# Optimization experiments

Hardware: AMD Instinct MI355X
Metric: run time of the kernel (lower is better)

## Reference

```python
import jax, jax.numpy as jnp
import numpy as np

MAX_FRAMES = 12
TOPK = 49
NUM_SAMPLES = 500
SIGMA = 0.05
EPS = 1e-5
NOISE_KEY = jax.random.key(1)


def _ln(x, g, b):
    m = x.mean(-1, keepdims=True)
    v = ((x - m) ** 2).mean(-1, keepdims=True)
    return (x - m) / jnp.sqrt(v + EPS) * g + b


def _gelu(x):
    return jax.nn.gelu(x, approximate=False)  # torch nn.GELU default is exact erf


def _predict(x, guid, ln_in_g, ln_in_b, W_in, ln_gd_g, ln_gd_b, W_gd, W_out1, W_out2):
    # x: (b, N, D), guid: (b, 1, D) -> score (b, N, 1)
    b, N, D = x.shape
    local = _gelu(_ln(x, ln_in_g, ln_in_b) @ W_in)            # (b, N, D/2)
    glob = _gelu(_ln(guid, ln_gd_g, ln_gd_b) @ W_gd)          # (b, 1, D/2); LN is per-token so repeat-then-LN == LN-then-broadcast
    glob = jnp.broadcast_to(glob, (b, N, glob.shape[-1]))
    h = jnp.concatenate([local, glob], axis=-1)               # (b, N, D)
    return jnp.tanh(_gelu(h @ W_out1) @ W_out2)               # (b, N, 1)


def _perturbed_topk(scores):
    # scores: (b, d) -> soft indicators (b, k, d); same math as one_hot(sorted topk idx).mean over samples,
    # computed by scatter-add instead of materializing the (b, ns, k, d) one-hot tensor.
    b, d = scores.shape
    noise = jax.random.normal(NOISE_KEY, (b, NUM_SAMPLES, d), scores.dtype)
    perturbed = scores[:, None, :] + SIGMA * noise            # (b, ns, d)
    _, idx = jax.lax.top_k(perturbed, TOPK)                   # (b, ns, k)
    idx = jnp.sort(idx, axis=-1)
    bi = jnp.arange(b)[:, None, None]
    ki = jnp.arange(TOPK)[None, None, :]
    ind = jnp.zeros((b, TOPK, d), scores.dtype).at[bi, ki, idx].add(1.0 / NUM_SAMPLES)
    return ind


def setup_inputs() -> dict:
    key = jax.random.key(0)
    ks = jax.random.split(key, 9)
    B, F, N, D = 8, MAX_FRAMES, 196, 512
    H = D // 2
    s = 0.02
    return {
        "x": jax.random.normal(ks[0], (B, F * N, D), jnp.float32),
        "guidance_frame": jax.random.normal(ks[1], (B, F, D), jnp.float32),
        "guidance_sentence": jax.random.normal(ks[2], (B, 1, D), jnp.float32),
        "ln_in_g": jnp.ones((D,), jnp.float32),
        "ln_in_b": jnp.zeros((D,), jnp.float32),
        "W_in": jax.random.normal(ks[3], (D, H), jnp.float32) * s,
        "ln_gd_g": jnp.ones((D,), jnp.float32),
        "ln_gd_b": jnp.zeros((D,), jnp.float32),
        "W_gd": jax.random.normal(ks[4], (D, H), jnp.float32) * s,
        "W_out1": jax.random.normal(ks[5], (D, H), jnp.float32) * s,
        "W_out2": jax.random.normal(ks[6], (H, 1), jnp.float32) * s,
    }


def reference(x, guidance_frame, guidance_sentence, ln_in_g, ln_in_b, W_in, ln_gd_g, ln_gd_b, W_gd, W_out1, W_out2):
    B, L, D = x.shape
    N = L // MAX_FRAMES
    xf = x.reshape(B * MAX_FRAMES, N, D)                       # (b', N, D)
    gf = guidance_frame.reshape(B * MAX_FRAMES, 1, D)
    gs = jnp.broadcast_to(guidance_sentence, (B, MAX_FRAMES, D)).reshape(B * MAX_FRAMES, 1, D)
    s1 = _predict(xf, gf, ln_in_g, ln_in_b, W_in, ln_gd_g, ln_gd_b, W_gd, W_out1, W_out2)[..., 0]
    s2 = _predict(xf, gs, ln_in_g, ln_in_b, W_in, ln_gd_g, ln_gd_b, W_gd, W_out1, W_out2)[..., 0]
    score = s1 + s2                                            # (b', N)
    ind = _perturbed_topk(score)                               # (b', k, N)
    selected = jnp.einsum('bkl,bld->bkd', ind, xf)             # (b', k, D)
    return selected.reshape(B, MAX_FRAMES, TOPK, D)
```

## Files before the change

### kernel.cpp

```cpp
#include <hip/hip_runtime.h>
#include <stdint.h>

#define DEV __device__ __forceinline__

#define BP 96
#define NTOK 196
#define DIM 512
#define HID 256
#define NS 500
#define TOPK 49
#define ROWS (BP * NTOK)
#define GBLK (ROWS / 32)
#define SPB 10
#define CNTSZ (TOPK * NTOK)
#define SPAD 260

typedef _Float16 f16x8 __attribute__((ext_vector_type(8)));
typedef float f32x4 __attribute__((ext_vector_type(4)));

DEV float gelu32(float v) {
  return 0.5f * v * (1.0f + erff(v * 0.70710678f));
}

DEV void threefry2x32(uint32_t x0, uint32_t x1, uint32_t& o0, uint32_t& o1) {
  const uint32_t k0 = 0u, k1 = 1u;
  const uint32_t k2 = 0x1BD11BDAu ^ k0 ^ k1;
  x0 += k0; x1 += k1;
#define TF_R(r) { x0 += x1; x1 = (x1 << (r)) | (x1 >> (32 - (r))); x1 ^= x0; }
  TF_R(13) TF_R(15) TF_R(26) TF_R(6)
  x0 += k1; x1 += k2 + 1u;
  TF_R(17) TF_R(29) TF_R(16) TF_R(24)
  x0 += k2; x1 += k0 + 2u;
  TF_R(13) TF_R(15) TF_R(26) TF_R(6)
  x0 += k0; x1 += k1 + 3u;
  TF_R(17) TF_R(29) TF_R(16) TF_R(24)
  x0 += k1; x1 += k2 + 4u;
  TF_R(13) TF_R(15) TF_R(26) TF_R(6)
  x0 += k2; x1 += k0 + 5u;
#undef TF_R
  o0 = x0; o1 = x1;
}

DEV float erfinv_xla(float x) {
  float w = -__logf(fmaf(-x, x, 1.0f));
  float ws = w - 2.5f;
  float ps = 2.81022636e-08f;
  ps = fmaf(ps, ws, 3.43273939e-07f);
  ps = fmaf(ps, ws, -3.5233877e-06f);
  ps = fmaf(ps, ws, -4.39150654e-06f);
  ps = fmaf(ps, ws, 0.00021858087f);
  ps = fmaf(ps, ws, -0.00125372503f);
  ps = fmaf(ps, ws, -0.00417768164f);
  ps = fmaf(ps, ws, 0.246640727f);
  ps = fmaf(ps, ws, 1.50140941f);
  float r = ps;
  if (__ballot(w >= 5.0f) != 0ull) {
    float wl = sqrtf(w) - 3.0f;
    float pl = -0.000200214257f;
    pl = fmaf(pl, wl, 0.000100950558f);
    pl = fmaf(pl, wl, 0.00134934322f);
    pl = fmaf(pl, wl, -0.00367342844f);
    pl = fmaf(pl, wl, 0.00573950773f);
    pl = fmaf(pl, wl, -0.0076224613f);
    pl = fmaf(pl, wl, 0.00943887047f);
    pl = fmaf(pl, wl, 1.00167406f);
    pl = fmaf(pl, wl, 2.83297682f);
    r = (w < 5.0f) ? ps : pl;
  }
  return r * x;
}

DEV float noise_at(unsigned g) {
  unsigned o0, o1;
  threefry2x32(0u, g, o0, o1);
  unsigned bits = o0 ^ o1;
  float f = __uint_as_float((bits >> 9) | 0x3f800000u) - 1.0f;
  float u = f * 2.0f - 0.99999994f;
  u = fmaxf(-0.99999994f, u);
  return 1.41421356f * erfinv_xla(u);
}

DEV size_t pack_idx(int k, int col) {
  int t = k >> 5, kg = (k >> 3) & 3, e = k & 7;
  return (((size_t)(t * 4 + kg) * 256) + col) * 8 + e;
}

#define PRE_GLOB 192
#define PRE_PREP 512
#define PRE_STATS (ROWS / 4)
__global__ __launch_bounds__(256) void k_pre(
    const float* __restrict__ gf, const float* __restrict__ gs,
    const float* __restrict__ lng, const float* __restrict__ lnb,
    const float* __restrict__ Wgd, const float* __restrict__ Wout1,
    float* __restrict__ cout,
    const float* __restrict__ Win,
    const float* __restrict__ g_in, const float* __restrict__ b_in,
    _Float16* __restrict__ Pgh, _Float16* __restrict__ Pgl,
    _Float16* __restrict__ P1h, _Float16* __restrict__ P1l,
    float* __restrict__ gwv, float* __restrict__ bwv,
    const float* __restrict__ x, float* __restrict__ stats) {
  const int bid = blockIdx.x;
  if (bid < PRE_GLOB) {
    int bq = bid >> 1, which = bid & 1;
    const float* row = which ? (gs + (size_t)(bq / 12) * DIM) : (gf + (size_t)bq * DIM);
    __shared__ float lx[DIM];
    __shared__ float sg[HID];
    __shared__ double sred[8];
    int tid = threadIdx.x, lane = tid & 63, wv = tid >> 6;
    float v0 = row[tid], v1 = row[tid + 256];
    double s = (double)v0 + v1, q = (double)v0 * v0 + (double)v1 * v1;
    #pragma unroll
    for (int m = 1; m < 64; m <<= 1) { s += __shfl_xor(s, m); q += __shfl_xor(q, m); }
    if (lane == 0) { sred[wv * 2] = s; sred[wv * 2 + 1] = q; }
    __syncthreads();
    double ts = sred[0] + sred[2] + sred[4] + sred[6];
    double tq = sred[1] + sred[3] + sred[5] + sred[7];
    double mean = ts / 512.0;
    double var = tq / 512.0 - mean * mean;
    float mn = (float)mean;
    float rs = (float)(1.0 / sqrt(var + 1e-5));
    lx[tid]       = (v0 - mn) * rs * lng[tid] + lnb[tid];
    lx[tid + 256] = (v1 - mn) * rs * lng[tid + 256] + lnb[tid + 256];
    __syncthreads();
    float acc = 0.0f;
    for (int d = 0; d < DIM; ++d) acc = fmaf(lx[d], Wgd[(size_t)d * HID + tid], acc);
    sg[tid] = gelu32(acc);
    __syncthreads();
    float c = 0.0f;
    for (int j = 0; j < HID; ++j) c = fmaf(sg[j], Wout1[(size_t)(HID + j) * HID + tid], c);
    cout[((size_t)which * BP + bq) * HID + tid] = c;
  } else if (bid < PRE_GLOB + PRE_PREP) {
    int b2 = bid - PRE_GLOB;
    int n = b2 & 255, half = b2 >> 8;
    if (half == 0) {
      __shared__ float wred[8];
      int tid = threadIdx.x, lane = tid & 63, wv = tid >> 6;
      float sgv = 0.0f, sbv = 0.0f;
      #pragma unroll
      for (int kk = 0; kk < 2; ++kk) {
        int k = tid + kk * 256;
        float w = Win[(size_t)k * HID + n];
        float wg = w * g_in[k];
        _Float16 h = (_Float16)wg;
        size_t pi = pack_idx(k, n);
        Pgh[pi] = h;
        Pgl[pi] = (_Float16)(wg - (float)h);
        sgv += wg;
        sbv = fmaf(b_in[k], w, sbv);
      }
      #pragma unroll
      for (int m = 1; m < 64; m <<= 1) { sgv += __shfl_xor(sgv, m); sbv += __shfl_xor(sbv, m); }
      if (lane == 0) { wred[wv * 2] = sgv; wred[wv * 2 + 1] = sbv; }
      __syncthreads();
      if (tid == 0) {
        gwv[n] = wred[0] + wred[2] + wred[4] + wred[6];
        bwv[n] = wred[1] + wred[3] + wred[5] + wred[7];
      }
    } else {
      int k = threadIdx.x;
      float v = Wout1[(size_t)k * HID + n];
      _Float16 h = (_Float16)v;
      size_t pi = pack_idx(k, n);
      P1h[pi] = h;
      P1l[pi] = (_Float16)(v - (float)h);
    }
  } else {
    int r = (bid - PRE_GLOB - PRE_PREP) * 4 + (threadIdx.x >> 6);
    int lane = threadIdx.x & 63;
    const float4* xr = (const float4*)(x + (size_t)r * DIM);
    float4 a = xr[lane], c = xr[lane + 64];
    double s = (double)a.x + a.y + a.z + a.w + (double)c.x + c.y + c.z + c.w;
    double q = (double)a.x * a.x + (double)a.y * a.y + (double)a.z * a.z + (double)a.w * a.w +
               (double)c.x * c.x + (double)c.y * c.y + (double)c.z * c.z + (double)c.w * c.w;
    #pragma unroll
    for (int m = 1; m < 64; m <<= 1) { s += __shfl_xor(s, m); q += __shfl_xor(q, m); }
    if (lane == 0) {
      double mean = s / 512.0;
      double var = q / 512.0 - mean * mean;
      stats[r * 2]     = (float)mean;
      stats[r * 2 + 1] = (float)(1.0 / sqrt(var + 1e-5));
    }
  }
}

#define LOADA(src0, src1, t, pb)                                               \
  {                                                                            \
    axv[pb][0] = *(const float4*)((src0) + (t) * 32);                          \
    axv[pb][1] = *(const float4*)((src0) + (t) * 32 + 4);                      \
    axv[pb][2] = *(const float4*)((src1) + (t) * 32);                          \
    axv[pb][3] = *(const float4*)((src1) + (t) * 32 + 4);                      \
  }

#define LOADA_LDS(t, pb)                                                       \
  {                                                                            \
    axv[pb][0] = *(const float4*)&stage[lr * SPAD + (t) * 32 + kg * 8];        \
    axv[pb][1] = *(const float4*)&stage[lr * SPAD + (t) * 32 + kg * 8 + 4];    \
    axv[pb][2] = *(const float4*)&stage[(16 + lr) * SPAD + (t) * 32 + kg * 8]; \
    axv[pb][3] = *(const float4*)&stage[(16 + lr) * SPAD + (t) * 32 + kg * 8 + 4]; \
  }

#define LOADB(bh, bl, t, pb)                                                   \
  {                                                                            \
    _Pragma("unroll")                                                          \
    for (int ni = 0; ni < 4; ++ni) {                                           \
      bxh[pb][ni] = *(const f16x8*)((bh) + (size_t)(t) * 8192 + ni * 128);     \
      bxl[pb][ni] = *(const f16x8*)((bl) + (size_t)(t) * 8192 + ni * 128);     \
    }                                                                          \
  }

#define SPLITA(pb, fah, fal)                                                   \
  {                                                                            \
    _Pragma("unroll")                                                          \
    for (int mi = 0; mi < 2; ++mi) {                                           \
      float va[8];                                                             \
      *(float4*)&va[0] = axv[pb][mi * 2];                                      \
      *(float4*)&va[4] = axv[pb][mi * 2 + 1];                                  \
      _Pragma("unroll")                                                        \
      for (int e = 0; e < 8; ++e) {                                            \
        _Float16 h = (_Float16)va[e];                                          \
        fah[mi][e] = h;                                                        \
        fal[mi][e] = (_Float16)(va[e] - (float)h);                             \
      }                                                                        \
    }                                                                          \
  }

#define MFMA_CHUNK(pb, fah, fal)                                               \
  {                                                                            \
    _Pragma("unroll")                                                          \
    for (int mi = 0; mi < 2; ++mi)                                             \
      _Pragma("unroll")                                                        \
      for (int ni = 0; ni < 4; ++ni) {                                         \
        acc[mi][ni] = __builtin_amdgcn_mfma_f32_16x16x32_f16(fah[mi], bxh[pb][ni], acc[mi][ni], 0, 0, 0); \
        acc[mi][ni] = __builtin_amdgcn_mfma_f32_16x16x32_f16(fah[mi], bxl[pb][ni], acc[mi][ni], 0, 0, 0); \
        acc[mi][ni] = __builtin_amdgcn_mfma_f32_16x16x32_f16(fal[mi], bxh[pb][ni], acc[mi][ni], 0, 0, 0); \
      }                                                                        \
  }

__global__ __launch_bounds__(256) void k_gemm(
    const float* __restrict__ x, const float* __restrict__ stats,
    const _Float16* __restrict__ Pgh, const _Float16* __restrict__ Pgl,
    const float* __restrict__ gwv, const float* __restrict__ bwv,
    const _Float16* __restrict__ P1h, const _Float16* __restrict__ P1l,
    const float* __restrict__ W2, const float* __restrict__ c1,
    const float* __restrict__ c2, float* __restrict__ scores) {
  __shared__ float stage[32 * SPAD];
  __shared__ float red1[32][4], red2[32][4];
  const int tid = threadIdx.x, lane = tid & 63, w = tid >> 6;
  const int kg = lane >> 4, lr = lane & 15;
  const int gr0 = blockIdx.x * 32;

  const float* asrc0 = x + (size_t)(gr0 + lr) * DIM + kg * 8;
  const float* asrc1 = x + (size_t)(gr0 + 16 + lr) * DIM + kg * 8;
  const _Float16* bh = Pgh + ((size_t)kg * 256 + w * 64 + lr) * 8;
  const _Float16* bl = Pgl + ((size_t)kg * 256 + w * 64 + lr) * 8;
  const _Float16* bh2 = P1h + ((size_t)kg * 256 + w * 64 + lr) * 8;
  const _Float16* bl2 = P1l + ((size_t)kg * 256 + w * 64 + lr) * 8;

  f32x4 acc[2][4];
  const f32x4 z4 = {0.f, 0.f, 0.f, 0.f};
  #pragma unroll
  for (int mi = 0; mi < 2; ++mi)
    #pragma unroll
    for (int ni = 0; ni < 4; ++ni) acc[mi][ni] = z4;
  float4 axv[2][4];
  f16x8 bxh[2][4], bxl[2][4];

  LOADA(asrc0, asrc1, 0, 0)
  LOADB(bh, bl, 0, 0)
  #pragma unroll
  for (int t = 0; t < 16; ++t) {
    const int pb = t & 1;
    if (t + 1 < 16) {
      LOADA(asrc0, asrc1, t + 1, pb ^ 1)
      LOADB(bh, bl, t + 1, pb ^ 1)
    }
    f16x8 fah[2], fal[2];
    SPLITA(pb, fah, fal)
    MFMA_CHUNK(pb, fah, fal)
  }

  {
    float gwc[4], bwc[4];
    #pragma unroll
    for (int ni = 0; ni < 4; ++ni) {
      int col = w * 64 + ni * 16 + lr;
      gwc[ni] = gwv[col];
      bwc[ni] = bwv[col];
    }
    #pragma unroll
    for (int mi = 0; mi < 2; ++mi)
      #pragma unroll
      for (int i = 0; i < 4; ++i) {
        int rrel = mi * 16 + kg * 4 + i;
        int row = gr0 + rrel;
        float mn = stats[row * 2], rs = stats[row * 2 + 1];
        #pragma unroll
        for (int ni = 0; ni < 4; ++ni) {
          int col = w * 64 + ni * 16 + lr;
          float v = rs * acc[mi][ni][i] - rs * mn * gwc[ni] + bwc[ni];
          stage[rrel * SPAD + col] = gelu32(v);
        }
      }
  }
  LOADB(bh2, bl2, 0, 0)
  __syncthreads();

  #pragma unroll
  for (int mi = 0; mi < 2; ++mi)
    #pragma unroll
    for (int ni = 0; ni < 4; ++ni) acc[mi][ni] = z4;
  LOADA_LDS(0, 0)
  #pragma unroll
  for (int t = 0; t < 8; ++t) {
    const int pb = t & 1;
    if (t + 1 < 8) {
      LOADA_LDS(t + 1, pb ^ 1)
      LOADB(bh2, bl2, t + 1, pb ^ 1)
    }
    f16x8 fah[2], fal[2];
    SPLITA(pb, fah, fal)
    MFMA_CHUNK(pb, fah, fal)
  }

  float w2v[4];
  #pragma unroll
  for (int ni = 0; ni < 4; ++ni) w2v[ni] = W2[w * 64 + ni * 16 + lr];
  #pragma unroll
  for (int mi = 0; mi < 2; ++mi) {
    #pragma unroll
    for (int i = 0; i < 4; ++i) {
      int row = gr0 + mi * 16 + kg * 4 + i;
      int bf = row / NTOK;
      float p1 = 0.f, p2 = 0.f;
      #pragma unroll
      for (int ni = 0; ni < 4; ++ni) {
        int col = w * 64 + ni * 16 + lr;
        float u = acc[mi][ni][i];
        p1 = fmaf(gelu32(u + c1[(size_t)bf * HID + col]), w2v[ni], p1);
        p2 = fmaf(gelu32(u + c2[(size_t)bf * HID + col]), w2v[ni], p2);
      }
      #pragma unroll
      for (int m = 1; m < 16; m <<= 1) { p1 += __shfl_xor(p1, m); p2 += __shfl_xor(p2, m); }
      if (lr == 0) {
        red1[mi * 16 + kg * 4 + i][w] = p1;
        red2[mi * 16 + kg * 4 + i][w] = p2;
      }
    }
  }
  __syncthreads();
  if (tid < 32) {
    float s1 = red1[tid][0] + red1[tid][1] + red1[tid][2] + red1[tid][3];
    float s2 = red2[tid][0] + red2[tid][1] + red2[tid][2] + red2[tid][3];
    scores[gr0 + tid] = tanhf(s1) + tanhf(s2);
  }
}

__global__ __launch_bounds__(512) void k_topk(const float* __restrict__ scores,
                                              unsigned short* __restrict__ partial) {
  const int b = blockIdx.x, chunk = blockIdx.y;
  const int tid = threadIdx.x, lane = tid & 63, wv = tid >> 6;
  __shared__ float sc_s[NTOK];
  __shared__ int cnt_s[CNTSZ];
  if (tid < NTOK) sc_s[tid] = scores[b * NTOK + tid];
  for (int i = tid; i < CNTSZ; i += 512) cnt_s[i] = 0;

  const int s_first = chunk + SPB * wv;
  const unsigned gb = (unsigned)b * NS * 196u;

  float n_tail = 0.0f;
  {
    int si = lane >> 2, t = lane & 3;
    int s = s_first + si * (SPB * 8);
    if (lane < 28 && s < NS) {
      n_tail = noise_at(gb + (unsigned)s * 196u + 192u + (unsigned)t);
    }
  }
  __syncthreads();

  int si = 0;
  for (int s = s_first; s < NS; s += SPB * 8, ++si) {
    const unsigned gbase = gb + (unsigned)s * 196u;
    unsigned key[4];
    #pragma unroll
    for (int c = 0; c < 3; ++c) {
      float n = noise_at(gbase + (unsigned)(c * 64 + lane));
      float p = fmaf(0.05f, n, sc_s[c * 64 + lane]);
      unsigned ub = __float_as_uint(p);
      key[c] = (ub & 0x80000000u) ? ~ub : (ub | 0x80000000u);
    }
    {
      float n = __shfl(n_tail, si * 4 + (lane & 3));
      float p = fmaf(0.05f, n, sc_s[192 + (lane & 3)]);
      unsigned ub = __float_as_uint(p);
      unsigned k3 = (ub & 0x80000000u) ? ~ub : (ub | 0x80000000u);
      key[3] = (lane < 4) ? k3 : 0u;
    }
    unsigned prefix = 0u;
    bool exact = false;
    for (int bit = 31; bit >= 0; --bit) {
      unsigned t = prefix | (1u << bit);
      int cn = 0;
      #pragma unroll
      for (int c = 0; c < 4; ++c) cn += __popcll(__ballot(key[c] >= t));
      if (cn >= TOPK) {
        prefix = t;
        if (cn == TOPK) { exact = true; break; }
      }
    }
    unsigned long long lt = (1ull << lane) - 1ull;
    bool sel[4];
    if (exact) {
      #pragma unroll
      for (int c = 0; c < 4; ++c) sel[c] = key[c] >= prefix;
    } else {
      unsigned long long mE[4];
      int cntG = 0;
      #pragma unroll
      for (int c = 0; c < 4; ++c) {
        cntG += __popcll(__ballot(key[c] > prefix));
        mE[c] = __ballot(key[c] == prefix);
      }
      int need = TOPK - cntG;
      #pragma unroll
      for (int c = 0; c < 4; ++c) {
        int er = 0;
        for (int cc = 0; cc < c; ++cc) er += __popcll(mE[cc]);
        er += __popcll(mE[c] & lt);
        sel[c] = (key[c] > prefix) || ((key[c] == prefix) && (er < need));
      }
    }
    unsigned long long mS[4];
    #pragma unroll
    for (int c = 0; c < 4; ++c) mS[c] = __ballot(sel[c]);
    int base = 0;
    #pragma unroll
    for (int c = 0; c < 4; ++c) {
      if (sel[c]) {
        int rank = base + __popcll(mS[c] & lt);
        int j = c * 64 + lane;
        atomicAdd(&cnt_s[rank * NTOK + j], 1);
      }
      base += __popcll(mS[c]);
    }
  }
  __syncthreads();
  unsigned short* dst = partial + ((size_t)b * SPB + chunk) * CNTSZ;
  for (int i = tid; i < CNTSZ; i += 512) dst[i] = (unsigned short)cnt_s[i];
}

__global__ __launch_bounds__(256) void k_out(const float* __restrict__ x,
                                             const unsigned short* __restrict__ partial,
                                             float* __restrict__ out) {
  int bid = blockIdx.x;
  int b = bid % BP, k = bid / BP;
  __shared__ float swv[NTOK];
  __shared__ int idxs[NTOK];
  __shared__ int wcnt[4];
  __shared__ int wbase[5];
  __shared__ float4 part2[128];
  const int tid = threadIdx.x, lane = tid & 63, wv = tid >> 6;

  int cval = 0;
  if (tid < NTOK) {
    #pragma unroll
    for (int cc = 0; cc < SPB; ++cc)
      cval += partial[((size_t)b * SPB + cc) * CNTSZ + k * NTOK + tid];
  }
  unsigned long long m = __ballot(cval != 0);
  if (lane == 0) wcnt[wv] = __popcll(m);
  __syncthreads();
  if (tid == 0) {
    int a = 0;
    #pragma unroll
    for (int i = 0; i < 4; ++i) { wbase[i] = a; a += wcnt[i]; }
    wbase[4] = a;
  }
  __syncthreads();
  if (cval != 0) {
    int pos = wbase[wv] + __popcll(m & ((1ull << lane) - 1ull));
    idxs[pos] = tid;
    swv[pos] = (float)cval * 0.002f;
  }
  __syncthreads();
  const int n = wbase[4];
  const int half = tid >> 7, d4 = tid & 127;
  const int i0 = half ? (n + 1) / 2 : 0;
  const int i1 = half ? n : (n + 1) / 2;
  float a0 = 0, a1 = 0, a2 = 0, a3 = 0;
  for (int i = i0; i < i1; ++i) {
    float w = swv[i];
    float4 xv = *(const float4*)(x + ((size_t)(b * NTOK + idxs[i])) * DIM + d4 * 4);
    a0 = fmaf(w, xv.x, a0); a1 = fmaf(w, xv.y, a1);
    a2 = fmaf(w, xv.z, a2); a3 = fmaf(w, xv.w, a3);
  }
  if (half == 1) part2[d4] = make_float4(a0, a1, a2, a3);
  __syncthreads();
  if (half == 0) {
    float4 p = part2[d4];
    float4 o = make_float4(a0 + p.x, a1 + p.y, a2 + p.z, a3 + p.w);
    *(float4*)(out + ((size_t)(b * TOPK + k)) * DIM + d4 * 4) = o;
  }
}

extern "C" void kernel_launch(void* const* d_in, const int* in_sizes, int n_in,
                              void* d_out, int out_size, void* d_ws, size_t ws_size,
                              hipStream_t stream) {
  const float* x       = (const float*)d_in[0];
  const float* gf      = (const float*)d_in[1];
  const float* gs      = (const float*)d_in[2];
  const float* ln_in_g = (const float*)d_in[3];
  const float* ln_in_b = (const float*)d_in[4];
  const float* W_in    = (const float*)d_in[5];
  const float* ln_gd_g = (const float*)d_in[6];
  const float* ln_gd_b = (const float*)d_in[7];
  const float* W_gd    = (const float*)d_in[8];
  const float* W_out1  = (const float*)d_in[9];
  const float* W_out2  = (const float*)d_in[10];
  float* out = (float*)d_out;

  char* p = (char*)d_ws;
  unsigned short* partial = (unsigned short*)p; p += (size_t)BP * SPB * CNTSZ * 2;
  float* stats   = (float*)p;             p += (size_t)ROWS * 2 * 4;
  float* c1      = (float*)p;             p += (size_t)BP * HID * 4;
  float* c2      = (float*)p;             p += (size_t)BP * HID * 4;
  float* scores  = (float*)p;             p += (size_t)ROWS * 4;
  _Float16* Pgh  = (_Float16*)p;          p += (size_t)HID * DIM * 2;
  _Float16* Pgl  = (_Float16*)p;          p += (size_t)HID * DIM * 2;
  _Float16* P1h  = (_Float16*)p;          p += (size_t)HID * HID * 2;
  _Float16* P1l  = (_Float16*)p;          p += (size_t)HID * HID * 2;
  float* gwv     = (float*)p;             p += HID * 4;
  float* bwv     = (float*)p;             p += HID * 4;

  k_pre<<<PRE_GLOB + PRE_PREP + PRE_STATS, 256, 0, stream>>>(
      gf, gs, ln_gd_g, ln_gd_b, W_gd, W_out1, c1,
      W_in, ln_in_g, ln_in_b, Pgh, Pgl, P1h, P1l, gwv, bwv, x, stats);
  k_gemm<<<GBLK, 256, 0, stream>>>(x, stats, Pgh, Pgl, gwv, bwv,
                                   P1h, P1l, W_out2, c1, c2, scores);
  k_topk<<<dim3(BP, SPB), 512, 0, stream>>>(scores, partial);
  k_out<<<BP * TOPK, 256, 0, stream>>>(x, partial, out);
}
```

Measured before the change: 154.8 us.

## Pre-split x into packed fp16 hi/lo tiles in prep kernel for GEMM

Adds a stage to the prep kernel that converts x into fp16 high/low halves laid out in the MFMA fragment order for each 32-row block. The first GEMM then loads ready-made f16x8 fragments instead of loading fp32 rows and splitting them in registers. This is meant to cut VALU conversion work and uncoalesced strided loads in the GEMM main loop. In exchange it writes and reads an extra 2x fp16 copy of x (the same byte count as x) through global memory, and it aliases the workspace region used by the top-k partial counts, which relies on stream ordering.

```diff
diff --git a/kernel.cpp b/kernel.cpp
--- a/kernel.cpp
+++ b/kernel.cpp
@@ -88,6 +88,7 @@
 #define PRE_GLOB 192
 #define PRE_PREP 512
 #define PRE_STATS (ROWS / 4)
+#define PRE_PACK (GBLK * 8)
 __global__ __launch_bounds__(256) void k_pre(
     const float* __restrict__ gf, const float* __restrict__ gs,
     const float* __restrict__ lng, const float* __restrict__ lnb,
@@ -98,7 +99,8 @@
     _Float16* __restrict__ Pgh, _Float16* __restrict__ Pgl,
     _Float16* __restrict__ P1h, _Float16* __restrict__ P1l,
     float* __restrict__ gwv, float* __restrict__ bwv,
-    const float* __restrict__ x, float* __restrict__ stats) {
+    const float* __restrict__ x, float* __restrict__ stats,
+    _Float16* __restrict__ xPh, _Float16* __restrict__ xPl) {
   const int bid = blockIdx.x;
   if (bid < PRE_GLOB) {
     int bq = bid >> 1, which = bid & 1;
@@ -164,7 +166,7 @@
       P1h[pi] = h;
       P1l[pi] = (_Float16)(v - (float)h);
     }
-  } else {
+  } else if (bid < PRE_GLOB + PRE_PREP + PRE_STATS) {
     int r = (bid - PRE_GLOB - PRE_PREP) * 4 + (threadIdx.x >> 6);
     int lane = threadIdx.x & 63;
     const float4* xr = (const float4*)(x + (size_t)r * DIM);
@@ -180,15 +182,46 @@
       stats[r * 2]     = (float)mean;
       stats[r * 2 + 1] = (float)(1.0 / sqrt(var + 1e-5));
     }
-  }
-}
-
-#define LOADA(src0, src1, t, pb)                                               \
+  } else {
+    int idx = bid - PRE_GLOB - PRE_PREP - PRE_STATS;
+    int rb = idx >> 3, cc = idx & 7;
+    __shared__ float cbuf[32][67];
+    const int tid = threadIdx.x;
+    {
+      int r = tid >> 3, c8 = (tid & 7) * 8;
+      const float* src = x + ((size_t)rb * 32 + r) * DIM + cc * 64 + c8;
+      float4 v0 = *(const float4*)src;
+      float4 v1 = *(const float4*)(src + 4);
+      *(float4*)&cbuf[r][c8] = v0;
+      *(float4*)&cbuf[r][c8 + 4] = v1;
+    }
+    __syncthreads();
+    {
+      int combo = tid >> 5;
+      int tloc = combo >> 2, kg = combo & 3;
+      int r = tid & 31;
+      int t = cc * 2 + tloc;
+      f16x8 h8, l8;
+      #pragma unroll
+      for (int e = 0; e < 8; ++e) {
+        float v = cbuf[r][tloc * 32 + kg * 8 + e];
+        _Float16 h = (_Float16)v;
+        h8[e] = h;
+        l8[e] = (_Float16)(v - (float)h);
+      }
+      size_t off = (size_t)rb * 16384 + (((size_t)t * 4 + kg) * 32 + r) * 8;
+      *(f16x8*)(xPh + off) = h8;
+      *(f16x8*)(xPl + off) = l8;
+    }
+  }
+}
+
+#define LOADAF(axh, axl, t, pb)                                                \
   {                                                                            \
-    axv[pb][0] = *(const float4*)((src0) + (t) * 32);                          \
-    axv[pb][1] = *(const float4*)((src0) + (t) * 32 + 4);                      \
-    axv[pb][2] = *(const float4*)((src1) + (t) * 32);                          \
-    axv[pb][3] = *(const float4*)((src1) + (t) * 32 + 4);                      \
+    fahb[pb][0] = *(const f16x8*)((axh) + (t) * 1024);                         \
+    fahb[pb][1] = *(const f16x8*)((axh) + (t) * 1024 + 128);                   \
+    falb[pb][0] = *(const f16x8*)((axl) + (t) * 1024);                         \
+    falb[pb][1] = *(const f16x8*)((axl) + (t) * 1024 + 128);                   \
   }
 
 #define LOADA_LDS(t, pb)                                                       \
@@ -224,7 +257,7 @@
     }                                                                          \
   }
 
-#define MFMA_CHUNK(pb, fah, fal)                                               \
+#define MFMA_CHUNK(fah, fal)                                                   \
   {                                                                            \
     _Pragma("unroll")                                                          \
     for (int mi = 0; mi < 2; ++mi)                                             \
@@ -237,7 +270,8 @@
   }
 
 __global__ __launch_bounds__(256) void k_gemm(
-    const float* __restrict__ x, const float* __restrict__ stats,
+    const _Float16* __restrict__ xPh, const _Float16* __restrict__ xPl,
+    const float* __restrict__ stats,
     const _Float16* __restrict__ Pgh, const _Float16* __restrict__ Pgl,
     const float* __restrict__ gwv, const float* __restrict__ bwv,
     const _Float16* __restrict__ P1h, const _Float16* __restrict__ P1l,
@@ -249,8 +283,8 @@
   const int kg = lane >> 4, lr = lane & 15;
   const int gr0 = blockIdx.x * 32;
 
-  const float* asrc0 = x + (size_t)(gr0 + lr) * DIM + kg * 8;
-  const float* asrc1 = x + (size_t)(gr0 + 16 + lr) * DIM + kg * 8;
+  const _Float16* axh = xPh + (size_t)blockIdx.x * 16384 + ((size_t)kg * 32 + lr) * 8;
+  const _Float16* axl = xPl + (size_t)blockIdx.x * 16384 + ((size_t)kg * 32 + lr) * 8;
   const _Float16* bh = Pgh + ((size_t)kg * 256 + w * 64 + lr) * 8;
   const _Float16* bl = Pgl + ((size_t)kg * 256 + w * 64 + lr) * 8;
   const _Float16* bh2 = P1h + ((size_t)kg * 256 + w * 64 + lr) * 8;
@@ -262,21 +296,19 @@
   for (int mi = 0; mi < 2; ++mi)
     #pragma unroll
     for (int ni = 0; ni < 4; ++ni) acc[mi][ni] = z4;
-  float4 axv[2][4];
+  f16x8 fahb[2][2], falb[2][2];
   f16x8 bxh[2][4], bxl[2][4];
 
-  LOADA(asrc0, asrc1, 0, 0)
+  LOADAF(axh, axl, 0, 0)
   LOADB(bh, bl, 0, 0)
   #pragma unroll
   for (int t = 0; t < 16; ++t) {
     const int pb = t & 1;
     if (t + 1 < 16) {
-      LOADA(asrc0, asrc1, t + 1, pb ^ 1)
+      LOADAF(axh, axl, t + 1, pb ^ 1)
       LOADB(bh, bl, t + 1, pb ^ 1)
     }
-    f16x8 fah[2], fal[2];
-    SPLITA(pb, fah, fal)
-    MFMA_CHUNK(pb, fah, fal)
+    MFMA_CHUNK(fahb[pb], falb[pb])
   }
 
   {
@@ -309,6 +341,7 @@
   for (int mi = 0; mi < 2; ++mi)
     #pragma unroll
     for (int ni = 0; ni < 4; ++ni) acc[mi][ni] = z4;
+  float4 axv[2][4];
   LOADA_LDS(0, 0)
   #pragma unroll
   for (int t = 0; t < 8; ++t) {
@@ -319,7 +352,7 @@
     }
     f16x8 fah[2], fal[2];
     SPLITA(pb, fah, fal)
-    MFMA_CHUNK(pb, fah, fal)
+    MFMA_CHUNK(fah, fal)
   }
 
   float w2v[4];
@@ -519,7 +552,10 @@
   float* out = (float*)d_out;
 
   char* p = (char*)d_ws;
-  unsigned short* partial = (unsigned short*)p; p += (size_t)BP * SPB * CNTSZ * 2;
+  _Float16* xPh = (_Float16*)p;
+  _Float16* xPl = xPh + (size_t)ROWS * DIM;
+  unsigned short* partial = (unsigned short*)p;
+  p += (size_t)ROWS * DIM * 2 * 2;
   float* stats   = (float*)p;             p += (size_t)ROWS * 2 * 4;
   float* c1      = (float*)p;             p += (size_t)BP * HID * 4;
   float* c2      = (float*)p;             p += (size_t)BP * HID * 4;
@@ -531,10 +567,10 @@
   float* gwv     = (float*)p;             p += HID * 4;
   float* bwv     = (float*)p;             p += HID * 4;
 
-  k_pre<<<PRE_GLOB + PRE_PREP + PRE_STATS, 256, 0, stream>>>(
+  k_pre<<<PRE_GLOB + PRE_PREP + PRE_STATS + PRE_PACK, 256, 0, stream>>>(
       gf, gs, ln_gd_g, ln_gd_b, W_gd, W_out1, c1,
-      W_in, ln_in_g, ln_in_b, Pgh, Pgl, P1h, P1l, gwv, bwv, x, stats);
-  k_gemm<<<GBLK, 256, 0, stream>>>(x, stats, Pgh, Pgl, gwv, bwv,
+      W_in, ln_in_g, ln_in_b, Pgh, Pgl, P1h, P1l, gwv, bwv, x, stats, xPh, xPl);
+  k_gemm<<<GBLK, 256, 0, stream>>>(xPh, xPl, stats, Pgh, Pgl, gwv, bwv,
                                    P1h, P1l, W_out2, c1, c2, scores);
   k_topk<<<dim3(BP, SPB), 512, 0, stream>>>(scores, partial);
   k_out<<<BP * TOPK, 256, 0, stream>>>(x, partial, out);
```

Measured after the change: 150.2 us. 1.03x faster.
